# Kernel tuning notes

Measured on AMD Instinct MI355X. Metric: run time of the kernel, lower is better.

Reference implementation:

```python
import jax, jax.numpy as jnp
import numpy as np

B = 16384
D = 1024          # entity_dim
N_LAYERS = 4
TEMPERATURE = 32.0  # sqrt(entity_dim)


def setup_inputs() -> dict:
    key = jax.random.key(0)
    ks = jax.random.split(key, 6)
    d2 = 2 * D
    scale = 1.0 / np.sqrt(d2)
    x1 = jax.random.normal(ks[0], (B, D), dtype=jnp.float32)
    x2 = jax.random.normal(ks[1], (B, D), dtype=jnp.float32)
    # stacked per-layer Linear(2D, 2D) params; torch Linear stores W as [out, in]
    Ws = jax.random.normal(ks[2], (N_LAYERS, d2, d2), dtype=jnp.float32) * scale
    bs = jax.random.normal(ks[3], (N_LAYERS, d2), dtype=jnp.float32) * scale
    W_last = jax.random.normal(ks[4], (D, d2), dtype=jnp.float32) * scale
    b_last = jax.random.normal(ks[5], (D,), dtype=jnp.float32) * scale
    return {"x1": x1, "x2": x2, "Ws": Ws, "bs": bs, "W_last": W_last, "b_last": b_last}


def reference(x1, x2, Ws, bs, W_last, b_last):
    # x: [B, 2, D]
    x = jnp.stack((x1, x2), axis=1)
    # attn: [B, 2, 2] -- tiny self-attention over the 2 tokens
    attn = jnp.einsum('bsd,btd->bst', x / TEMPERATURE, x)
    attn = jax.nn.softmax(attn, axis=-1)  # dropout = identity in eval mode
    x = jnp.einsum('bst,btd->bsd', attn, x)
    # concat the two attended tokens -> [B, 2D]
    h = jnp.concatenate((x[:, 0, :], x[:, 1, :]), axis=-1)
    for i in range(N_LAYERS):
        h = jax.nn.relu(h @ Ws[i].T + bs[i])
    return h @ W_last.T + b_last
```

## Files before the change

### kernel.cpp

```cpp
#include <hip/hip_runtime.h>

typedef __bf16 bf16x8 __attribute__((ext_vector_type(8)));
typedef float f32x4 __attribute__((ext_vector_type(4)));

__device__ __forceinline__ unsigned short f2bf(float f) {
    unsigned int u = __builtin_bit_cast(unsigned int, f);
    u += 0x7FFFu + ((u >> 16) & 1u);
    return (unsigned short)(u >> 16);
}

__global__ void cvt_kernel(const float* __restrict__ in,
                           unsigned short* __restrict__ out, long n4) {
    long i = (long)blockIdx.x * blockDim.x + threadIdx.x;
    long stride = (long)gridDim.x * blockDim.x;
    for (; i < n4; i += stride) {
        float4 v = ((const float4*)in)[i];
        ushort4 o;
        o.x = f2bf(v.x); o.y = f2bf(v.y); o.z = f2bf(v.z); o.w = f2bf(v.w);
        ((ushort4*)out)[i] = o;
    }
}

__global__ __launch_bounds__(256) void attn_kernel(
    const float* __restrict__ x1, const float* __restrict__ x2,
    unsigned short* __restrict__ h) {
    const int D = 1024;
    const int lane = threadIdx.x & 63;
    const int wave = threadIdx.x >> 6;
    const long row = (long)blockIdx.x * 4 + wave;
    const float4* p1 = (const float4*)(x1 + row * D);
    const float4* p2 = (const float4*)(x2 + row * D);
    float4 v1[4], v2[4];
    float s11 = 0.f, s12 = 0.f, s22 = 0.f;
#pragma unroll
    for (int j = 0; j < 4; ++j) {
        v1[j] = p1[lane + 64 * j];
        v2[j] = p2[lane + 64 * j];
        s11 += v1[j].x * v1[j].x + v1[j].y * v1[j].y + v1[j].z * v1[j].z + v1[j].w * v1[j].w;
        s12 += v1[j].x * v2[j].x + v1[j].y * v2[j].y + v1[j].z * v2[j].z + v1[j].w * v2[j].w;
        s22 += v2[j].x * v2[j].x + v2[j].y * v2[j].y + v2[j].z * v2[j].z + v2[j].w * v2[j].w;
    }
#pragma unroll
    for (int off = 1; off < 64; off <<= 1) {
        s11 += __shfl_xor(s11, off);
        s12 += __shfl_xor(s12, off);
        s22 += __shfl_xor(s22, off);
    }
    const float a00 = 1.f / (1.f + expf((s12 - s11) * (1.f / 32.f)));
    const float a10 = 1.f / (1.f + expf((s22 - s12) * (1.f / 32.f)));
    const float a01 = 1.f - a00, a11 = 1.f - a10;
    unsigned short* h0 = h + row * 2048;
#pragma unroll
    for (int j = 0; j < 4; ++j) {
        const int f = lane + 64 * j;
        ushort4 o0, o1;
        o0.x = f2bf(a00 * v1[j].x + a01 * v2[j].x);
        o0.y = f2bf(a00 * v1[j].y + a01 * v2[j].y);
        o0.z = f2bf(a00 * v1[j].z + a01 * v2[j].z);
        o0.w = f2bf(a00 * v1[j].w + a01 * v2[j].w);
        o1.x = f2bf(a10 * v1[j].x + a11 * v2[j].x);
        o1.y = f2bf(a10 * v1[j].y + a11 * v2[j].y);
        o1.z = f2bf(a10 * v1[j].z + a11 * v2[j].z);
        o1.w = f2bf(a10 * v1[j].w + a11 * v2[j].w);
        ((ushort4*)(h0))[f] = o0;
        ((ushort4*)(h0 + 1024))[f] = o1;
    }
}

#define BAR   __builtin_amdgcn_s_barrier()
#define VMW0  asm volatile("s_waitcnt vmcnt(0)" ::: "memory")
#define PRIO1 __builtin_amdgcn_s_setprio(1)
#define PRIO0 __builtin_amdgcn_s_setprio(0)

#define MM03(kk, AR)                                                           \
  _Pragma("unroll") for (int n = 0; n < 4; ++n)                                \
  _Pragma("unroll") for (int mq = 0; mq < 4; ++mq)                             \
    acc[mq][n] = __builtin_amdgcn_mfma_f32_16x16x32_bf16(                      \
        Bf[n][kk], AR[mq], acc[mq][n], 0, 0, 0);
#define MM47(kk, AR)                                                           \
  _Pragma("unroll") for (int n = 0; n < 4; ++n)                                \
  _Pragma("unroll") for (int mq = 0; mq < 4; ++mq)                             \
    acc[4 + mq][n] = __builtin_amdgcn_mfma_f32_16x16x32_bf16(                  \
        Bf[n][kk], AR[mq], acc[4 + mq][n], 0, 0, 0);

template <bool RELU, typename OT>
__global__ __launch_bounds__(512, 2) void gemm256(
    const unsigned short* __restrict__ A,
    const unsigned short* __restrict__ Bw,
    const float* __restrict__ bias,
    OT* __restrict__ C,
    int N, int K) {
    __shared__ __align__(16) unsigned short lds[65536];
    const int tid = threadIdx.x;
    const int lane = tid & 63, wave = tid >> 6;
    const int wm = wave >> 2, wn = wave & 3;
    const int fr = lane & 15, fq = lane >> 4;

    const int cpx = (int)gridDim.x >> 3;
    const int swz = ((int)blockIdx.x & 7) * cpx + ((int)blockIdx.x >> 3);
    const int bm = swz & 63;
    const int bn = swz >> 6;
    const long m0 = (long)bm * 256, n0 = (long)bn * 256;

    const int x0 = fq ^ (fr & 7);
    const int lane_base = fr * 128 + x0 * 16;
    const int aBase = wm * 16384 + lane_base;
    const int bBase = 32768 + (wn >> 1) * 16384 + (wn & 1) * 8192 + lane_base;
    const char* ldsc = (const char*)lds;

    const int l3 = lane >> 3, l7 = lane & 7;
    const long rowb = (long)K * 2;
    const long lane_src = (long)l3 * rowb + ((l7 ^ l3) << 4);
    const char* Abl = (const char*)A + m0 * rowb + lane_src;
    const char* Bbl = (const char*)Bw + n0 * rowb + lane_src;

    auto stage = [&](const char* mb, int matOff, int hf, int kt, int T) {
#pragma unroll
        for (int r = 0; r < 2; ++r) {
            const int W = r * 8 + wave;
            const char* src = mb + (long)(hf * 128 + W * 8) * rowb + kt * 128;
            __builtin_amdgcn_global_load_lds(
                (const __attribute__((address_space(1))) void*)src,
                (__attribute__((address_space(3))) void*)((char*)lds +
                    (T * 65536 + matOff + hf * 16384 + W * 1024)),
                16, 0, 0);
        }
    };

    f32x4 acc[8][4] = {};
    bf16x8 Bf[4][2], Ap[4], Aq[4];

    auto rdB = [&](int boff, int kk) {
#pragma unroll
        for (int n = 0; n < 4; ++n)
            Bf[n][kk] = *(const bf16x8*)(ldsc + boff + (bBase ^ (kk << 6)) + n * 2048);
    };
    auto rdA03 = [&](int boff, int kk, bf16x8 (&D)[4]) {
#pragma unroll
        for (int m = 0; m < 4; ++m)
            D[m] = *(const bf16x8*)(ldsc + boff + (aBase ^ (kk << 6)) + m * 2048);
    };
    auto rdA47 = [&](int boff, int kk, bf16x8 (&D)[4]) {
#pragma unroll
        for (int m = 0; m < 4; ++m)
            D[m] = *(const bf16x8*)(ldsc + boff + (aBase ^ (kk << 6)) + (m + 4) * 2048);
    };

    stage(Abl, 0,     0, 0, 0); stage(Abl, 0,     1, 0, 0);
    stage(Bbl, 32768, 0, 0, 0); stage(Bbl, 32768, 1, 0, 0);
    VMW0;
    BAR;
    rdB(0, 0); rdA03(0, 0, Ap);

    const int NT = K >> 6;
    const int NIT = NT >> 1;
    for (int i = 0; i < NIT; ++i) {
        const int o = 2 * i + 1, e2 = 2 * i + 2;
        const bool g = (i + 1 < NIT);

        rdB(0, 1); rdA03(0, 1, Aq);
        stage(Abl, 0, 0, o, 1); stage(Abl, 0, 1, o, 1);
        PRIO1; MM03(0, Ap); PRIO0; BAR;

        rdA47(0, 0, Ap);
        stage(Bbl, 32768, 0, o, 1); stage(Bbl, 32768, 1, o, 1);
        PRIO1; MM03(1, Aq); PRIO0; BAR;

        rdA47(0, 1, Aq);
        PRIO1; MM47(0, Ap); PRIO0; BAR;

        VMW0; BAR;
        rdB(65536, 0); rdA03(65536, 0, Ap);
        PRIO1; MM47(1, Aq); PRIO0; BAR;

        rdB(65536, 1); rdA03(65536, 1, Aq);
        if (g) { stage(Abl, 0, 0, e2, 0); stage(Abl, 0, 1, e2, 0); }
        PRIO1; MM03(0, Ap); PRIO0; BAR;

        rdA47(65536, 0, Ap);
        if (g) { stage(Bbl, 32768, 0, e2, 0); stage(Bbl, 32768, 1, e2, 0); }
        PRIO1; MM03(1, Aq); PRIO0; BAR;

        rdA47(65536, 1, Aq);
        PRIO1; MM47(0, Ap); PRIO0; BAR;

        VMW0; BAR;
        if (g) { rdB(0, 0); rdA03(0, 0, Ap); }
        PRIO1; MM47(1, Aq); PRIO0; BAR;
    }

    const long crow0 = m0 + wm * 128 + fr;
    const long ccol0 = n0 + wn * 64 + fq * 4;
    float4 bv[4];
#pragma unroll
    for (int n = 0; n < 4; ++n) bv[n] = *(const float4*)(bias + ccol0 + n * 16);
#pragma unroll
    for (int m = 0; m < 8; ++m) {
        const long rb = (crow0 + m * 16) * N;
#pragma unroll
        for (int n = 0; n < 4; ++n) {
            float v0 = acc[m][n][0] + bv[n].x;
            float v1 = acc[m][n][1] + bv[n].y;
            float v2 = acc[m][n][2] + bv[n].z;
            float v3 = acc[m][n][3] + bv[n].w;
            if (RELU) {
                v0 = v0 > 0.f ? v0 : 0.f; v1 = v1 > 0.f ? v1 : 0.f;
                v2 = v2 > 0.f ? v2 : 0.f; v3 = v3 > 0.f ? v3 : 0.f;
            }
            if constexpr (sizeof(OT) == 2) {
                uint2 oo;
                oo.x = (unsigned)f2bf(v0) | ((unsigned)f2bf(v1) << 16);
                oo.y = (unsigned)f2bf(v2) | ((unsigned)f2bf(v3) << 16);
                *(uint2*)((unsigned short*)C + rb + ccol0 + n * 16) = oo;
            } else {
                *(float4*)((float*)C + rb + ccol0 + n * 16) =
                    make_float4(v0, v1, v2, v3);
            }
        }
    }
}

extern "C" void kernel_launch(void* const* d_in, const int* in_sizes, int n_in,
                              void* d_out, int out_size, void* d_ws, size_t ws_size,
                              hipStream_t stream) {
    const float* x1 = (const float*)d_in[0];
    const float* x2 = (const float*)d_in[1];
    const float* Ws = (const float*)d_in[2];
    const float* bs = (const float*)d_in[3];
    const float* Wl = (const float*)d_in[4];
    const float* bl = (const float*)d_in[5];
    float* out = (float*)d_out;

    char* ws = (char*)d_ws;
    unsigned short* hA  = (unsigned short*)(ws);
    unsigned short* hB  = (unsigned short*)(ws + (67108864L));
    unsigned short* Wbf = (unsigned short*)(ws + (134217728L));
    unsigned short* Wlb = (unsigned short*)(ws + (167772160L));

    cvt_kernel<<<2048, 256, 0, stream>>>(Ws, Wbf, 4L * 2048 * 2048 / 4);
    cvt_kernel<<<512, 256, 0, stream>>>(Wl, Wlb, 1024L * 2048 / 4);

    attn_kernel<<<16384 / 4, 256, 0, stream>>>(x1, x2, hA);

    gemm256<true, unsigned short><<<512, 512, 0, stream>>>(hA, Wbf + 0L * 2048 * 2048, bs + 0 * 2048, hB, 2048, 2048);
    gemm256<true, unsigned short><<<512, 512, 0, stream>>>(hB, Wbf + 1L * 2048 * 2048, bs + 1 * 2048, hA, 2048, 2048);
    gemm256<true, unsigned short><<<512, 512, 0, stream>>>(hA, Wbf + 2L * 2048 * 2048, bs + 2 * 2048, hB, 2048, 2048);
    gemm256<true, unsigned short><<<512, 512, 0, stream>>>(hB, Wbf + 3L * 2048 * 2048, bs + 3 * 2048, hA, 2048, 2048);
    gemm256<false, float><<<256, 512, 0, stream>>>(hA, Wlb, bl, out, 1024, 2048);
}
```

Baseline: 726.8 us.

## Restructure GEMM LDS layout into k-halves with deeper async prefetch pipeline

Changes the shared-memory tile layout to split each 64-wide K tile into two 32-wide halves with a new XOR swizzle, and reorganizes the main loop into eight phases that each stage one half-tile of A or B. Loads for tile t+2/t+3 are issued while tiles t/t+1 are computed, and partial vmcnt waits (vmcnt(6)) replace full drains. The intent is to keep more global→LDS loads in flight and hide latency behind MFMAs. In exchange it adds extra barriers and lgkmcnt waits per phase, and the more complex staging order carries some risk of correctness or hazard issues.

```diff
diff --git a/kernel.cpp b/kernel.cpp
--- a/kernel.cpp
+++ b/kernel.cpp
@@ -68,20 +68,17 @@
 }
 
 #define BAR   __builtin_amdgcn_s_barrier()
+#define LGKM0 asm volatile("s_waitcnt lgkmcnt(0)" ::: "memory")
+#define VMW6  asm volatile("s_waitcnt vmcnt(6)" ::: "memory")
 #define VMW0  asm volatile("s_waitcnt vmcnt(0)" ::: "memory")
 #define PRIO1 __builtin_amdgcn_s_setprio(1)
 #define PRIO0 __builtin_amdgcn_s_setprio(0)
 
-#define MM03(kk, AR)                                                           \
+#define MMQ(mb)                                                                \
   _Pragma("unroll") for (int n = 0; n < 4; ++n)                                \
   _Pragma("unroll") for (int mq = 0; mq < 4; ++mq)                             \
-    acc[mq][n] = __builtin_amdgcn_mfma_f32_16x16x32_bf16(                      \
-        Bf[n][kk], AR[mq], acc[mq][n], 0, 0, 0);
-#define MM47(kk, AR)                                                           \
-  _Pragma("unroll") for (int n = 0; n < 4; ++n)                                \
-  _Pragma("unroll") for (int mq = 0; mq < 4; ++mq)                             \
-    acc[4 + mq][n] = __builtin_amdgcn_mfma_f32_16x16x32_bf16(                  \
-        Bf[n][kk], AR[mq], acc[4 + mq][n], 0, 0, 0);
+    acc[(mb) + mq][n] = __builtin_amdgcn_mfma_f32_16x16x32_bf16(               \
+        Bf[n], Af[mq], acc[(mb) + mq][n], 0, 0, 0);
 
 template <bool RELU, typename OT>
 __global__ __launch_bounds__(512, 2) void gemm256(
@@ -101,92 +98,95 @@
     const int bm = swz & 63;
     const int bn = swz >> 6;
     const long m0 = (long)bm * 256, n0 = (long)bn * 256;
-
-    const int x0 = fq ^ (fr & 7);
-    const int lane_base = fr * 128 + x0 * 16;
-    const int aBase = wm * 16384 + lane_base;
-    const int bBase = 32768 + (wn >> 1) * 16384 + (wn & 1) * 8192 + lane_base;
+    const long rowb = (long)K * 2;
+
+    const int flip = ((fr >> 3) & 1) << 5;
+    const int lbase = fr * 64 + ((fq * 16) ^ flip);
+    const int aRd = wm * 8192 + lbase;
+    const int bRd = 32768 + wn * 4096 + lbase;
     const char* ldsc = (const char*)lds;
 
-    const int l3 = lane >> 3, l7 = lane & 7;
-    const long rowb = (long)K * 2;
-    const long lane_src = (long)l3 * rowb + ((l7 ^ l3) << 4);
-    const char* Abl = (const char*)A + m0 * rowb + lane_src;
-    const char* Bbl = (const char*)Bw + n0 * rowb + lane_src;
-
-    auto stage = [&](const char* mb, int matOff, int hf, int kt, int T) {
-#pragma unroll
-        for (int r = 0; r < 2; ++r) {
-            const int W = r * 8 + wave;
-            const char* src = mb + (long)(hf * 128 + W * 8) * rowb + kt * 128;
+    const int srow = wave * 16 + (lane >> 2);
+    const int scol = ((lane & 3) << 4) ^ ((lane >> 5) << 5);
+    const char* Abl = (const char*)A + m0 * rowb;
+    const char* Bbl = (const char*)Bw + n0 * rowb;
+
+    auto stage = [&](const char* mb, int regbase, int kh, int kt) {
+#pragma unroll
+        for (int L = 0; L < 2; ++L) {
+            const int r = L * 128 + srow;
+            const char* src = mb + (long)r * rowb + kt * 128 + kh * 64 + scol;
             __builtin_amdgcn_global_load_lds(
                 (const __attribute__((address_space(1))) void*)src,
                 (__attribute__((address_space(3))) void*)((char*)lds +
-                    (T * 65536 + matOff + hf * 16384 + W * 1024)),
+                    (regbase + kh * 16384 + L * 8192 + wave * 1024)),
                 16, 0, 0);
         }
     };
 
     f32x4 acc[8][4] = {};
-    bf16x8 Bf[4][2], Ap[4], Aq[4];
-
-    auto rdB = [&](int boff, int kk) {
-#pragma unroll
-        for (int n = 0; n < 4; ++n)
-            Bf[n][kk] = *(const bf16x8*)(ldsc + boff + (bBase ^ (kk << 6)) + n * 2048);
+    bf16x8 Bf[4], Af[4];
+
+    auto rdB = [&](int Tb, int kh) {
+        const int b = Tb + kh * 16384 + bRd;
+#pragma unroll
+        for (int nf = 0; nf < 4; ++nf)
+            Bf[nf] = *(const bf16x8*)(ldsc + b + nf * 1024);
     };
-    auto rdA03 = [&](int boff, int kk, bf16x8 (&D)[4]) {
-#pragma unroll
-        for (int m = 0; m < 4; ++m)
-            D[m] = *(const bf16x8*)(ldsc + boff + (aBase ^ (kk << 6)) + m * 2048);
+    auto rdA = [&](int Tb, int kh, int mh) {
+        const int b = Tb + kh * 16384 + aRd + mh * 4096;
+#pragma unroll
+        for (int mq = 0; mq < 4; ++mq)
+            Af[mq] = *(const bf16x8*)(ldsc + b + mq * 1024);
     };
-    auto rdA47 = [&](int boff, int kk, bf16x8 (&D)[4]) {
-#pragma unroll
-        for (int m = 0; m < 4; ++m)
-            D[m] = *(const bf16x8*)(ldsc + boff + (aBase ^ (kk << 6)) + (m + 4) * 2048);
-    };
-
-    stage(Abl, 0,     0, 0, 0); stage(Abl, 0,     1, 0, 0);
-    stage(Bbl, 32768, 0, 0, 0); stage(Bbl, 32768, 1, 0, 0);
-    VMW0;
+
+    stage(Bbl, 32768, 0, 0); stage(Abl, 0, 0, 0);
+    stage(Bbl, 32768, 1, 0); stage(Abl, 0, 1, 0);
+    stage(Bbl, 65536 + 32768, 0, 1); stage(Abl, 65536, 0, 1);
+    stage(Bbl, 65536 + 32768, 1, 1);
+    VMW6;
     BAR;
-    rdB(0, 0); rdA03(0, 0, Ap);
-
-    const int NT = K >> 6;
-    const int NIT = NT >> 1;
+
+    const int NT = K >> 6, NIT = NT >> 1;
     for (int i = 0; i < NIT; ++i) {
-        const int o = 2 * i + 1, e2 = 2 * i + 2;
+        const int u = 2 * i + 1, t2 = 2 * i + 2, t3 = 2 * i + 3;
         const bool g = (i + 1 < NIT);
 
-        rdB(0, 1); rdA03(0, 1, Aq);
-        stage(Abl, 0, 0, o, 1); stage(Abl, 0, 1, o, 1);
-        PRIO1; MM03(0, Ap); PRIO0; BAR;
-
-        rdA47(0, 0, Ap);
-        stage(Bbl, 32768, 0, o, 1); stage(Bbl, 32768, 1, o, 1);
-        PRIO1; MM03(1, Aq); PRIO0; BAR;
-
-        rdA47(0, 1, Aq);
-        PRIO1; MM47(0, Ap); PRIO0; BAR;
-
-        VMW0; BAR;
-        rdB(65536, 0); rdA03(65536, 0, Ap);
-        PRIO1; MM47(1, Aq); PRIO0; BAR;
-
-        rdB(65536, 1); rdA03(65536, 1, Aq);
-        if (g) { stage(Abl, 0, 0, e2, 0); stage(Abl, 0, 1, e2, 0); }
-        PRIO1; MM03(0, Ap); PRIO0; BAR;
-
-        rdA47(65536, 0, Ap);
-        if (g) { stage(Bbl, 32768, 0, e2, 0); stage(Bbl, 32768, 1, e2, 0); }
-        PRIO1; MM03(1, Aq); PRIO0; BAR;
-
-        rdA47(65536, 1, Aq);
-        PRIO1; MM47(0, Ap); PRIO0; BAR;
-
-        VMW0; BAR;
-        if (g) { rdB(0, 0); rdA03(0, 0, Ap); }
-        PRIO1; MM47(1, Aq); PRIO0; BAR;
+        rdB(0, 0); rdA(0, 0, 0);
+        stage(Abl, 65536, 1, u);
+        BAR; LGKM0; PRIO1; MMQ(0); PRIO0; BAR;
+
+        rdA(0, 0, 1);
+        if (g) stage(Bbl, 32768, 0, t2);
+        BAR; LGKM0; PRIO1; MMQ(4); PRIO0; BAR;
+
+        rdB(0, 1); rdA(0, 1, 0);
+        if (g) stage(Abl, 0, 0, t2);
+        BAR; LGKM0; PRIO1; MMQ(0); PRIO0; BAR;
+
+        rdA(0, 1, 1);
+        if (g) stage(Bbl, 32768, 1, t2);
+        BAR; LGKM0; PRIO1; MMQ(4); PRIO0;
+        if (g) { VMW6; } else { VMW0; }
+        BAR;
+
+        rdB(65536, 0); rdA(65536, 0, 0);
+        if (g) stage(Abl, 0, 1, t2);
+        BAR; LGKM0; PRIO1; MMQ(0); PRIO0; BAR;
+
+        rdA(65536, 0, 1);
+        if (g) stage(Bbl, 65536 + 32768, 0, t3);
+        BAR; LGKM0; PRIO1; MMQ(4); PRIO0; BAR;
+
+        rdB(65536, 1); rdA(65536, 1, 0);
+        if (g) stage(Abl, 65536, 0, t3);
+        BAR; LGKM0; PRIO1; MMQ(0); PRIO0; BAR;
+
+        rdA(65536, 1, 1);
+        if (g) stage(Bbl, 65536 + 32768, 1, t3);
+        BAR; LGKM0; PRIO1; MMQ(4); PRIO0;
+        if (g) { VMW6; } else { VMW0; }
+        BAR;
     }
 
     const long crow0 = m0 + wm * 128 + fr;
```

Result: faster. 672.4 us (-7.5%).
